# Kernel optimization log

Measured on AMD Instinct MI355X. Metric: run time of the kernel, lower is better.

## Reference

```python
import jax, jax.numpy as jnp
import numpy as np

BATCH, N, DIM_IN, DIM_K, DIM_V, NH = 2, 4096, 256, 256, 256, 8

def setup_inputs() -> dict:
    key = jax.random.key(0)
    k1, k2, k3, k4 = jax.random.split(key, 4)
    s = 1.0 / np.sqrt(DIM_IN)
    return {
        "x": jax.random.normal(k1, (BATCH, N, DIM_IN), dtype=jnp.float32),
        "Wq": jax.random.normal(k2, (DIM_IN, DIM_K), dtype=jnp.float32) * s,
        "Wk": jax.random.normal(k3, (DIM_IN, DIM_K), dtype=jnp.float32) * s,
        "Wv": jax.random.normal(k4, (DIM_IN, DIM_V), dtype=jnp.float32) * s,
    }

def reference(x, Wq, Wk, Wv):
    b, n, _ = x.shape
    nh = NH
    dk = DIM_K // nh
    dv = DIM_V // nh
    # project and split heads: [b, nh, n, dk]
    q = jnp.einsum('bni,ik->bnk', x, Wq).reshape(b, n, nh, dk).transpose(0, 2, 1, 3)
    k = jnp.einsum('bni,ik->bnk', x, Wk).reshape(b, n, nh, dk).transpose(0, 2, 1, 3)
    v = jnp.einsum('bni,iv->bnv', x, Wv).reshape(b, n, nh, dv).transpose(0, 2, 1, 3)
    scale = 1.0 / np.sqrt(dk)
    dist = jnp.einsum('bhqd,bhkd->bhqk', q, k) * scale  # [b, nh, n, n]
    dist = jax.nn.softmax(dist, axis=-1)
    # dropout is identity in eval mode
    att = jnp.einsum('bhqk,bhkv->bhqv', dist, v)  # [b, nh, n, dv]
    return att.transpose(0, 2, 1, 3).reshape(b, n, DIM_V)
```

## Files before the change

kernel.cpp:

```cpp
#include <hip/hip_runtime.h>
#include <math.h>

#define BATCH 2
#define SEQ   4096
#define DIN   256
#define NH    8
#define DH    32
#define BH    (BATCH*NH)
#define NSPLIT 4
#define KRANGE (SEQ/NSPLIT)
#define TILES  (KRANGE/64)
#define QTILE  256

typedef short bf16x8 __attribute__((ext_vector_type(8)));
typedef float f32x4  __attribute__((ext_vector_type(4)));

#if defined(__has_builtin)
#if __has_builtin(__builtin_amdgcn_exp2f)
#define EXP2(x) __builtin_amdgcn_exp2f(x)
#else
#define EXP2_ASM 1
#endif
#else
#define EXP2_ASM 1
#endif
#ifdef EXP2_ASM
__device__ __forceinline__ float exp2_raw(float x) {
    float r;
    asm("v_exp_f32 %0, %1\n\ts_nop 1" : "=v"(r) : "v"(x));
    return r;
}
#define EXP2(x) exp2_raw(x)
#endif

#define SC2 0.25508218f

__device__ __forceinline__ unsigned short f2bf(float f) {
    unsigned int u = __builtin_bit_cast(unsigned int, f);
    u += 0x7fffu + ((u >> 16) & 1u);
    return (unsigned short)(u >> 16);
}

__device__ __forceinline__ unsigned int pack_bf2(float f0, float f1) {
    unsigned int u0 = __builtin_bit_cast(unsigned int, f0) + 0x8000u;
    unsigned int u1 = __builtin_bit_cast(unsigned int, f1) + 0x8000u;
    return __builtin_amdgcn_perm(u1, u0, 0x07060302u);
}

__device__ __forceinline__ unsigned int pack_bf2_t(float f0, float f1) {
    return __builtin_amdgcn_perm(__builtin_bit_cast(unsigned int, f1),
                                 __builtin_bit_cast(unsigned int, f0),
                                 0x07060302u);
}

#if defined(__has_builtin)
#if __has_builtin(__builtin_amdgcn_global_load_lds)
#define HAS_ASYNC_LDS 1
#endif
#endif

__device__ __forceinline__ void stage16(const unsigned short* g,
                                        unsigned short* lds_base, int lane) {
#ifdef HAS_ASYNC_LDS
    __builtin_amdgcn_global_load_lds(
        (const __attribute__((address_space(1))) unsigned int*)g,
        (__attribute__((address_space(3))) unsigned int*)lds_base, 16, 0, 0);
#else
    *(bf16x8*)(lds_base + (size_t)lane * 8) = *(const bf16x8*)g;
#endif
}

__global__ __launch_bounds__(256) void prep_kernel(
    const float* __restrict__ x,
    const float* __restrict__ Wq, const float* __restrict__ Wk, const float* __restrict__ Wv,
    unsigned short* __restrict__ Wt, unsigned short* __restrict__ xb)
{
    __shared__ float ws[64][65];
    if (blockIdx.x >= 48) {
        int gid = (blockIdx.x - 48) * 256 + threadIdx.x;
        const float4* xs = (const float4*)x;
        float4 a = xs[(size_t)gid * 2];
        float4 b = xs[(size_t)gid * 2 + 1];
        uint4 p = { pack_bf2(a.x, a.y), pack_bf2(a.z, a.w),
                    pack_bf2(b.x, b.y), pack_bf2(b.z, b.w) };
        ((uint4*)xb)[gid] = p;
        return;
    }
    const int t = threadIdx.x;
    int wsel = blockIdx.x >> 4;
    int tile = blockIdx.x & 15;
    int tr = (tile >> 2) * 64;
    int tc = (tile & 3) * 64;
    const float* __restrict__ W = (wsel == 0) ? Wq : (wsel == 1) ? Wk : Wv;
    #pragma unroll
    for (int i = 0; i < 16; i++) {
        int row = i * 4 + (t >> 6), col = t & 63;
        ws[row][col] = W[(size_t)(tr + row) * DIN + tc + col];
    }
    __syncthreads();
    unsigned short* dst = Wt + (size_t)wsel * DIN * DIN;
    #pragma unroll
    for (int i = 0; i < 16; i++) {
        int orow = i * 4 + (t >> 6), ocol = t & 63;
        dst[(size_t)(tc + orow) * DIN + tr + ocol] = f2bf(ws[ocol][orow]);
    }
}

__global__ __launch_bounds__(256) void proj_kernel(
    const unsigned short* __restrict__ xb, const unsigned short* __restrict__ Wt,
    unsigned short* __restrict__ qh, unsigned short* __restrict__ kh,
    unsigned short* __restrict__ vt)
{
    __shared__ __align__(16) unsigned short abuf[8][4][64][8];
    __shared__ __align__(16) unsigned short bbuf[8][4][64][8];

    const int wsel = blockIdx.y;
    const int w    = threadIdx.x >> 6;
    const int lane = threadIdx.x & 63;
    const int quad = lane >> 4;
    const int l16  = lane & 15;

    const int sl   = lane ^ (lane >> 3);
    const int sl16 = sl >> 2, squad = sl & 3;
    const int s_ = (l16 << 2) | quad;
    const int jj = (s_ & 56) | ((s_ ^ (s_ >> 3)) & 7);

    int arow0, brow0;
    const unsigned short* Wbase;
    const unsigned short* Xbase;
    unsigned short (*wdst)[4][64][8];
    unsigned short (*xdst)[4][64][8];
    if (wsel < 2) {
        int tt = blockIdx.x >> 7, nt = blockIdx.x & 127;
        arow0 = tt * 64; brow0 = nt * 64;
        Wbase = Wt + (size_t)wsel * DIN * DIN + (size_t)arow0 * DIN;
        Xbase = xb + (size_t)brow0 * DIN;
        wdst = abuf; xdst = bbuf;
    } else {
        int nt = blockIdx.x >> 2, tt = blockIdx.x & 3;
        arow0 = nt * 64; brow0 = tt * 64;
        Xbase = xb + (size_t)arow0 * DIN;
        Wbase = Wt + (size_t)2 * DIN * DIN + (size_t)brow0 * DIN;
        wdst = bbuf; xdst = abuf;
    }

    #pragma unroll
    for (int i = 0; i < 8; i++) {
        int id = w * 8 + i;
        int kb = id >> 2, rt = id & 3;
        stage16(Wbase + (size_t)(rt * 16 + sl16) * DIN + kb * 32 + squad * 8,
                &wdst[kb][rt][0][0], lane);
    }
    #pragma unroll
    for (int i = 0; i < 8; i++) {
        int id = w * 8 + i;
        int kb = id >> 2, rt = id & 3;
        stage16(Xbase + (size_t)(rt * 16 + sl16) * DIN + kb * 32 + squad * 8,
                &xdst[kb][rt][0][0], lane);
    }
    __syncthreads();

    f32x4 acc[4];
    #pragma unroll
    for (int c = 0; c < 4; c++) acc[c] = (f32x4){0.f, 0.f, 0.f, 0.f};
    #pragma unroll
    for (int kb = 0; kb < 8; kb++) {
        bf16x8 af = *(const bf16x8*)&abuf[kb][w][jj][0];
        #pragma unroll
        for (int c = 0; c < 4; c++) {
            bf16x8 bfr = *(const bf16x8*)&bbuf[kb][c][jj][0];
            acc[c] = __builtin_amdgcn_mfma_f32_16x16x32_bf16(af, bfr, acc[c], 0, 0, 0);
        }
    }

    if (wsel < 2) {
        const float scl = (wsel == 0) ? SC2 : 1.0f;
        unsigned short* __restrict__ dst0 = (wsel == 0) ? qh : kh;
        const int t0 = arow0 + w * 16;
        const int h = t0 >> 5, d0 = (t0 & 31) + quad * 4;
        #pragma unroll
        for (int c = 0; c < 4; c++) {
            int n = brow0 + c * 16 + l16;
            int b = n >> 12, n12 = n & 4095;
            unsigned int u01 = pack_bf2(acc[c][0] * scl, acc[c][1] * scl);
            unsigned int u23 = pack_bf2(acc[c][2] * scl, acc[c][3] * scl);
            *(uint2*)&dst0[((size_t)(b * NH + h) * SEQ + n12) * DH + d0] = make_uint2(u01, u23);
        }
    } else {
        const int n0w = arow0 + w * 16;
        const int b = n0w >> 12, nbase = (n0w & 4095) + quad * 4;
        #pragma unroll
        for (int c = 0; c < 4; c++) {
            int t = brow0 + c * 16;
            int h = t >> 5, d = (t & 31) + l16;
            unsigned int u01 = pack_bf2(acc[c][0], acc[c][1]);
            unsigned int u23 = pack_bf2(acc[c][2], acc[c][3]);
            *(uint2*)&vt[((size_t)(b * NH + h) * DH + d) * SEQ + nbase] = make_uint2(u01, u23);
        }
    }
}

__global__ __launch_bounds__(256, 4) void attn_kernel(
    const unsigned short* __restrict__ qh,
    const unsigned short* __restrict__ kh,
    const unsigned short* __restrict__ vt,
    unsigned short* __restrict__ po, float* __restrict__ pl)
{
    __shared__ __align__(16) unsigned short pbuf[4][2][16][64];
    __shared__ __align__(16) unsigned short kbuf[2][4][64][8];
    __shared__ __align__(16) unsigned short vbuf[2][4][64][8];

    const int tid  = threadIdx.x;
    const int wave = tid >> 6;
    const int lane = tid & 63;
    const int quad = lane >> 4;
    const int l16  = lane & 15;
    const int sw   = l16 & 7;

    const int bh = blockIdx.x & 15;
    const int qb = (blockIdx.x >> 4) & 15;
    const int ks = blockIdx.x >> 8;
    const int q0 = qb * QTILE + wave * 64;
    const int kbase = ks * KRANGE;

    const unsigned short* __restrict__ Qp = qh + (size_t)bh * SEQ * DH;
    const unsigned short* __restrict__ Kp = kh + (size_t)bh * SEQ * DH;
    const unsigned short* __restrict__ Vp = vt + (size_t)bh * DH * SEQ;

    const int sl    = lane ^ (lane >> 3);
    const int sl16  = sl >> 2, squad = sl & 3;
    const unsigned short* ksrc = Kp + (size_t)(kbase + wave * 16 + sl16) * DH + squad * 8;
    const int vdh = wave >> 1, vkh = wave & 1;
    const unsigned short* vsrc = Vp + (size_t)(vdh * 16 + sl16) * SEQ + kbase + vkh * 32 + squad * 8;

    const int s_ = (l16 << 2) | quad;
    const int jj = (s_ & 56) | ((s_ ^ (s_ >> 3)) & 7);

    bf16x8 qf[4];
    #pragma unroll
    for (int i = 0; i < 4; i++)
        qf[i] = *(const bf16x8*)(Qp + (size_t)(q0 + i * 16 + l16) * DH + quad * 8);

    const bf16x8 ones = {0x3F80, 0x3F80, 0x3F80, 0x3F80,
                         0x3F80, 0x3F80, 0x3F80, 0x3F80};

    f32x4 o[4][2];
    f32x4 lones[4];
    #pragma unroll
    for (int i = 0; i < 4; i++) {
        o[i][0] = (f32x4){0.f, 0.f, 0.f, 0.f};
        o[i][1] = (f32x4){0.f, 0.f, 0.f, 0.f};
        lones[i] = (f32x4){0.f, 0.f, 0.f, 0.f};
    }
    const f32x4 z = {0.f, 0.f, 0.f, 0.f};

    stage16(ksrc, &kbuf[0][wave][0][0], lane);
    stage16(vsrc, &vbuf[0][wave][0][0], lane);
    ksrc += 64 * DH;
    vsrc += 64;

    for (int t = 0; t < TILES; t++) {
        const int buf = t & 1;

        __syncthreads();

        if (t + 1 < TILES) {
            stage16(ksrc, &kbuf[buf ^ 1][wave][0][0], lane);
            stage16(vsrc, &vbuf[buf ^ 1][wave][0][0], lane);
            ksrc += 64 * DH;
            vsrc += 64;
        }

        bf16x8 kf[4], vf[4];
        #pragma unroll
        for (int c = 0; c < 4; c++) kf[c] = *(const bf16x8*)&kbuf[buf][c][jj][0];
        #pragma unroll
        for (int f = 0; f < 4; f++) vf[f] = *(const bf16x8*)&vbuf[buf][f][jj][0];

        #pragma unroll
        for (int qt = 0; qt < 4; qt++) {
            const int pr = qt & 1;
            #pragma unroll
            for (int c = 0; c < 4; c++) {
                f32x4 s = __builtin_amdgcn_mfma_f32_16x16x32_bf16(kf[c], qf[qt], z, 0, 0, 0);
                float e0 = EXP2(s[0]);
                float e1 = EXP2(s[1]);
                float e2 = EXP2(s[2]);
                float e3 = EXP2(s[3]);
                int chs = ((c * 2 + (quad >> 1)) ^ sw) * 8 + (quad & 1) * 4;
                *(uint2*)&pbuf[wave][pr][l16][chs] =
                    make_uint2(pack_bf2_t(e0, e1), pack_bf2_t(e2, e3));
            }
            bf16x8 pf0 = *(const bf16x8*)&pbuf[wave][pr][l16][((0 + quad) ^ sw) * 8];
            bf16x8 pf1 = *(const bf16x8*)&pbuf[wave][pr][l16][((4 + quad) ^ sw) * 8];
            __builtin_amdgcn_s_setprio(1);
            o[qt][0] = __builtin_amdgcn_mfma_f32_16x16x32_bf16(pf0, vf[0], o[qt][0], 0, 0, 0);
            o[qt][0] = __builtin_amdgcn_mfma_f32_16x16x32_bf16(pf1, vf[1], o[qt][0], 0, 0, 0);
            o[qt][1] = __builtin_amdgcn_mfma_f32_16x16x32_bf16(pf0, vf[2], o[qt][1], 0, 0, 0);
            o[qt][1] = __builtin_amdgcn_mfma_f32_16x16x32_bf16(pf1, vf[3], o[qt][1], 0, 0, 0);
            lones[qt] = __builtin_amdgcn_mfma_f32_16x16x32_bf16(pf0, ones, lones[qt], 0, 0, 0);
            lones[qt] = __builtin_amdgcn_mfma_f32_16x16x32_bf16(pf1, ones, lones[qt], 0, 0, 0);
            __builtin_amdgcn_s_setprio(0);
        }
    }

    const size_t obase = (size_t)(ks * BH + bh) * SEQ;
    #pragma unroll
    for (int qt = 0; qt < 4; qt++) {
        if (l16 == 0) {
            #pragma unroll
            for (int r = 0; r < 4; r++)
                pl[obase + q0 + qt * 16 + quad * 4 + r] = lones[qt][r];
        }
        #pragma unroll
        for (int r = 0; r < 4; r++) {
            int n = q0 + qt * 16 + quad * 4 + r;
            unsigned short* dst = po + (obase + n) * DH;
            dst[l16]      = f2bf(o[qt][0][r]);
            dst[16 + l16] = f2bf(o[qt][1][r]);
        }
    }
}

__global__ __launch_bounds__(256) void merge_kernel(
    const unsigned short* __restrict__ po, const float* __restrict__ pl,
    float* __restrict__ out)
{
    int t    = blockIdx.x * 256 + threadIdx.x;
    int d8   = t & 7;
    int pair = t >> 3;
    int bh   = pair >> 12;
    int n    = pair & 4095;
    float s0 = 0.f, s1 = 0.f, s2 = 0.f, s3 = 0.f, ls = 0.f;
    #pragma unroll
    for (int sp = 0; sp < NSPLIT; sp++) {
        size_t base = (size_t)(sp * BH + bh) * SEQ + n;
        uint2 v = ((const uint2*)(po + base * DH))[d8];
        s0 += __builtin_bit_cast(float, v.x << 16);
        s1 += __builtin_bit_cast(float, v.x & 0xFFFF0000u);
        s2 += __builtin_bit_cast(float, v.y << 16);
        s3 += __builtin_bit_cast(float, v.y & 0xFFFF0000u);
        ls += pl[base];
    }
    float inv = 1.f / ls;
    int b = bh >> 3, h = bh & 7;
    float4 o = {s0 * inv, s1 * inv, s2 * inv, s3 * inv};
    ((float4*)(out + ((size_t)b * SEQ + n) * (NH * DH) + h * DH))[d8] = o;
}

extern "C" void kernel_launch(void* const* d_in, const int* in_sizes, int n_in,
                              void* d_out, int out_size, void* d_ws, size_t ws_size,
                              hipStream_t stream)
{
    const float* x  = (const float*)d_in[0];
    const float* Wq = (const float*)d_in[1];
    const float* Wk = (const float*)d_in[2];
    const float* Wv = (const float*)d_in[3];
    float* out = (float*)d_out;

    unsigned short* qh = (unsigned short*)d_ws;
    unsigned short* kh = qh + (size_t)BH * SEQ * DH;
    unsigned short* vt = kh + (size_t)BH * SEQ * DH;
    unsigned short* Wt = vt + (size_t)BH * SEQ * DH;
    unsigned short* po = Wt + 3 * DIN * DIN;
    float* pl = (float*)(po + (size_t)NSPLIT * BH * SEQ * DH);
    unsigned short* xb = (unsigned short*)(pl + (size_t)NSPLIT * BH * SEQ);

    prep_kernel<<<dim3(48 + 1024), 256, 0, stream>>>(x, Wq, Wk, Wv, Wt, xb);
    proj_kernel<<<dim3(512, 3), 256, 0, stream>>>(xb, Wt, qh, kh, vt);
    attn_kernel<<<dim3(BH * (SEQ / QTILE) * NSPLIT), 256, 0, stream>>>(qh, kh, vt, po, pl);
    merge_kernel<<<dim3(2048), 256, 0, stream>>>(po, pl, out);
}
```

Before: 131.9 us.

## Fuse split-K merge into attention kernel via last-block atomic counter

Removes the separate merge kernel launch. Each attention block bumps a per-(bh, q-tile) atomic counter after writing its partial output and row sum, and the last of the NSPLIT blocks reduces all partials and writes the final output. The counters are zeroed by an extra block in the prep kernel. This saves a kernel launch and lets the merge overlap with other attention blocks, at the cost of fences, atomics, and a serialized merge tail inside some blocks.

```diff
diff --git a/kernel.cpp b/kernel.cpp
--- a/kernel.cpp
+++ b/kernel.cpp
@@ -73,9 +73,14 @@
 __global__ __launch_bounds__(256) void prep_kernel(
     const float* __restrict__ x,
     const float* __restrict__ Wq, const float* __restrict__ Wk, const float* __restrict__ Wv,
-    unsigned short* __restrict__ Wt, unsigned short* __restrict__ xb)
+    unsigned short* __restrict__ Wt, unsigned short* __restrict__ xb,
+    unsigned int* __restrict__ cnt)
 {
     __shared__ float ws[64][65];
+    if (blockIdx.x == 48 + 1024) {
+        cnt[threadIdx.x] = 0u;
+        return;
+    }
     if (blockIdx.x >= 48) {
         int gid = (blockIdx.x - 48) * 256 + threadIdx.x;
         const float4* xs = (const float4*)x;
@@ -204,7 +209,8 @@
     const unsigned short* __restrict__ qh,
     const unsigned short* __restrict__ kh,
     const unsigned short* __restrict__ vt,
-    unsigned short* __restrict__ po, float* __restrict__ pl)
+    unsigned short* __restrict__ po, float* __restrict__ pl,
+    unsigned int* __restrict__ cnt, float* __restrict__ out)
 {
     __shared__ __align__(16) unsigned short pbuf[4][2][16][64];
     __shared__ __align__(16) unsigned short kbuf[2][4][64][8];
@@ -320,32 +326,38 @@
             dst[16 + l16] = f2bf(o[qt][1][r]);
         }
     }
-}
-
-__global__ __launch_bounds__(256) void merge_kernel(
-    const unsigned short* __restrict__ po, const float* __restrict__ pl,
-    float* __restrict__ out)
-{
-    int t    = blockIdx.x * 256 + threadIdx.x;
-    int d8   = t & 7;
-    int pair = t >> 3;
-    int bh   = pair >> 12;
-    int n    = pair & 4095;
-    float s0 = 0.f, s1 = 0.f, s2 = 0.f, s3 = 0.f, ls = 0.f;
-    #pragma unroll
-    for (int sp = 0; sp < NSPLIT; sp++) {
-        size_t base = (size_t)(sp * BH + bh) * SEQ + n;
-        uint2 v = ((const uint2*)(po + base * DH))[d8];
-        s0 += __builtin_bit_cast(float, v.x << 16);
-        s1 += __builtin_bit_cast(float, v.x & 0xFFFF0000u);
-        s2 += __builtin_bit_cast(float, v.y << 16);
-        s3 += __builtin_bit_cast(float, v.y & 0xFFFF0000u);
-        ls += pl[base];
-    }
-    float inv = 1.f / ls;
-    int b = bh >> 3, h = bh & 7;
-    float4 o = {s0 * inv, s1 * inv, s2 * inv, s3 * inv};
-    ((float4*)(out + ((size_t)b * SEQ + n) * (NH * DH) + h * DH))[d8] = o;
+
+    __threadfence();
+    __syncthreads();
+    __shared__ unsigned int lastflag;
+    if (tid == 0) {
+        unsigned int old = atomicAdd(&cnt[bh * 16 + qb], 1u);
+        lastflag = (old == NSPLIT - 1) ? 1u : 0u;
+    }
+    __syncthreads();
+    if (lastflag) {
+        __threadfence();
+        const int d8 = tid & 7;
+        const int b = bh >> 3, h = bh & 7;
+        #pragma unroll
+        for (int pass = 0; pass < 8; pass++) {
+            int n = qb * QTILE + pass * 32 + (tid >> 3);
+            float s0 = 0.f, s1 = 0.f, s2 = 0.f, s3 = 0.f, ls = 0.f;
+            #pragma unroll
+            for (int sp = 0; sp < NSPLIT; sp++) {
+                size_t base = (size_t)(sp * BH + bh) * SEQ + n;
+                uint2 v = ((const uint2*)(po + base * DH))[d8];
+                s0 += __builtin_bit_cast(float, v.x << 16);
+                s1 += __builtin_bit_cast(float, v.x & 0xFFFF0000u);
+                s2 += __builtin_bit_cast(float, v.y << 16);
+                s3 += __builtin_bit_cast(float, v.y & 0xFFFF0000u);
+                ls += pl[base];
+            }
+            float inv = 1.f / ls;
+            float4 ov = {s0 * inv, s1 * inv, s2 * inv, s3 * inv};
+            ((float4*)(out + ((size_t)b * SEQ + n) * (NH * DH) + h * DH))[d8] = ov;
+        }
+    }
 }
 
 extern "C" void kernel_launch(void* const* d_in, const int* in_sizes, int n_in,
@@ -365,9 +377,9 @@
     unsigned short* po = Wt + 3 * DIN * DIN;
     float* pl = (float*)(po + (size_t)NSPLIT * BH * SEQ * DH);
     unsigned short* xb = (unsigned short*)(pl + (size_t)NSPLIT * BH * SEQ);
-
-    prep_kernel<<<dim3(48 + 1024), 256, 0, stream>>>(x, Wq, Wk, Wv, Wt, xb);
+    unsigned int* cnt = (unsigned int*)(xb + (size_t)BATCH * SEQ * DIN);
+
+    prep_kernel<<<dim3(48 + 1024 + 1), 256, 0, stream>>>(x, Wq, Wk, Wv, Wt, xb, cnt);
     proj_kernel<<<dim3(512, 3), 256, 0, stream>>>(xb, Wt, qh, kh, vt);
-    attn_kernel<<<dim3(BH * (SEQ / QTILE) * NSPLIT), 256, 0, stream>>>(qh, kh, vt, po, pl);
-    merge_kernel<<<dim3(2048), 256, 0, stream>>>(po, pl, out);
-}
+    attn_kernel<<<dim3(BH * (SEQ / QTILE) * NSPLIT), 256, 0, stream>>>(qh, kh, vt, po, pl, cnt, out);
+}
```

After: 276.6 us. 110% more time.
